# Optimization experiments

Hardware: AMD Instinct MI355X
Metric: run time of the kernel (lower is better)

## Reference

```python
import jax, jax.numpy as jnp
import numpy as np

NUM_HEADS = 16
NUM_GROUPS = 4
EPS = 1e-6


def _rope_tables(seq_len, head_dim):
    inv_freq = 1.0 / (10000.0 ** (jnp.arange(0, head_dim, 2, dtype=jnp.float32) / head_dim))
    t = jnp.arange(seq_len, dtype=jnp.float32)
    freqs = jnp.outer(t, inv_freq)  # [s, hd//2]
    return jnp.sin(freqs), jnp.cos(freqs)


def _apply_rope(x, sin, cos):
    # x: [b, s, h, hd]; sin/cos: [s, hd//2] -> broadcast over batch and heads
    sin = sin[None, :, None, :]
    cos = cos[None, :, None, :]
    x1 = x[..., ::2]
    x2 = x[..., 1::2]
    out1 = x1 * cos - x2 * sin
    out2 = x1 * sin + x2 * cos
    return jnp.stack([out1, out2], axis=-1).reshape(x.shape).astype(x.dtype)


def _rmsnorm(x, scale):
    var = jnp.mean(jnp.square(x), axis=-1, keepdims=True)
    return x * jax.lax.rsqrt(var + EPS) * scale


def setup_inputs() -> dict:
    key = jax.random.key(0)
    b, s, d = 16, 512, 2048
    hd = d // NUM_HEADS
    g = NUM_GROUPS
    ks = jax.random.split(key, 9)
    std = 0.02
    return {
        "x": jax.random.normal(ks[0], (b, s, d), dtype=jnp.float32),
        "Wq": jax.random.normal(ks[1], (d, d), dtype=jnp.float32) * std,
        "bq": jnp.zeros((d,), dtype=jnp.float32),
        "Wk": jax.random.normal(ks[2], (d, g * hd), dtype=jnp.float32) * std,
        "bk": jnp.zeros((g * hd,), dtype=jnp.float32),
        "Wv": jax.random.normal(ks[3], (d, g * hd), dtype=jnp.float32) * std,
        "bv": jnp.zeros((g * hd,), dtype=jnp.float32),
        "Wo": jax.random.normal(ks[4], (d, d), dtype=jnp.float32) * std,
        "bo": jnp.zeros((d,), dtype=jnp.float32),
        "q_norm_scale": jnp.ones((hd,), dtype=jnp.float32),
        "k_norm_scale": jnp.ones((hd,), dtype=jnp.float32),
    }


def reference(x, Wq, bq, Wk, bk, Wv, bv, Wo, bo, q_norm_scale, k_norm_scale):
    b, s, d = x.shape
    H, G = NUM_HEADS, NUM_GROUPS
    hd = d // H
    P = H // G  # queries per kv group
    inv_sqrt_hd = hd ** (-0.5)

    q = (x @ Wq + bq).reshape(b, s, H, hd)
    k = (x @ Wk + bk).reshape(b, s, G, hd)
    v = (x @ Wv + bv).reshape(b, s, G, hd)

    q = _rmsnorm(q, q_norm_scale)
    k = _rmsnorm(k, k_norm_scale)

    sin, cos = _rope_tables(s, hd)
    q = _apply_rope(q, sin, cos) * inv_sqrt_hd  # module pre-scales q
    k = _apply_rope(k, sin, cos)

    # GQA attention with causal mask; dot_product_attention applies an
    # additional 1/sqrt(hd) scale on top of the module's pre-scaling.
    qg = q.reshape(b, s, G, P, hd)
    logits = jnp.einsum("bsgph,btgh->bgpst", qg, k) * inv_sqrt_hd
    causal = jnp.tril(jnp.ones((s, s), dtype=bool))
    logits = jnp.where(causal[None, None, None, :, :], logits, jnp.finfo(logits.dtype).min)
    attn = jax.nn.softmax(logits, axis=-1)
    out = jnp.einsum("bgpst,btgh->bsgph", attn, v).reshape(b, s, d)
    return out @ Wo + bo
```

## Files before the change

kernel.cpp:

```cpp
#include <hip/hip_runtime.h>
#include <stdint.h>

typedef __attribute__((ext_vector_type(4))) float floatx4;
typedef __attribute__((ext_vector_type(16))) float floatx16;
typedef __attribute__((ext_vector_type(8))) short short8;

#define BB 16
#define SS 512
#define DD 2048
#define HH_ 16
#define HD 128
#define GG 4
#define MM (BB*SS)
#define NQKV 3072

__device__ __forceinline__ unsigned short f2bf(float f){
  unsigned u = __builtin_bit_cast(unsigned, f);
  u += 0x7fffu + ((u >> 16) & 1u);
  return (unsigned short)(u >> 16);
}
__device__ __forceinline__ float bf2f_lo(unsigned d){
  return __builtin_bit_cast(float, d << 16);
}
__device__ __forceinline__ float bf2f_hi(unsigned d){
  return __builtin_bit_cast(float, d & 0xffff0000u);
}

__device__ __forceinline__ void async_copy16(const void* g, void* l){
  __builtin_amdgcn_global_load_lds((const __attribute__((address_space(1))) unsigned*)g,
                                   (__attribute__((address_space(3))) unsigned*)l,
                                   16, 0, 0);
}

#define PB_CVT   16384
#define PB_TRQ   (PB_CVT + 4096)
#define PB_TRK   (PB_TRQ + 1024)
#define PB_TRV   (PB_TRK + 1024)
#define PB_TRO   (PB_TRV + 4096)
#define PB_ALL   (PB_TRO + 12)

__global__ __launch_bounds__(256) void prep_kernel(
    const float* __restrict__ x,
    const float* __restrict__ Wq, const float* __restrict__ Wk,
    const float* __restrict__ Wv, const float* __restrict__ Wo,
    const float* __restrict__ bq, const float* __restrict__ bk,
    const float* __restrict__ bv,
    unsigned short* __restrict__ xb, unsigned short* __restrict__ WqkvT,
    unsigned short* __restrict__ WoT, float* __restrict__ bqkv)
{
  __shared__ float tile[32][33];
  const int bid = blockIdx.x, tid = threadIdx.x;

  if (bid < PB_CVT) {
    const int i = bid * 256 + tid;
    float4 f = ((const float4*)x)[i];
    ushort4 o;
    o.x = f2bf(f.x); o.y = f2bf(f.y); o.z = f2bf(f.z); o.w = f2bf(f.w);
    ((ushort4*)xb)[i] = o;
    return;
  }
  if (bid < PB_TRO) {
    const float* src; unsigned short* dst; int R, C, b2;
    if (bid < PB_TRQ)      { src = Wq; dst = WqkvT;                          R = 2048; C = 2048; b2 = bid - PB_CVT; }
    else if (bid < PB_TRK) { src = Wk; dst = WqkvT + (size_t)2048 * 2048;    R = 2048; C = 512;  b2 = bid - PB_TRQ; }
    else if (bid < PB_TRV) { src = Wv; dst = WqkvT + (size_t)2560 * 2048;    R = 2048; C = 512;  b2 = bid - PB_TRK; }
    else                   { src = Wo; dst = WoT;                            R = 2048; C = 2048; b2 = bid - PB_TRV; }
    const int nbx = C >> 5;
    const int c0 = (b2 % nbx) * 32, r0 = (b2 / nbx) * 32;
    const int tx = tid & 31, ty = tid >> 5;
    #pragma unroll
    for (int j = 0; j < 32; j += 8)
      tile[ty + j][tx] = src[(size_t)(r0 + ty + j) * C + (c0 + tx)];
    __syncthreads();
    #pragma unroll
    for (int j = 0; j < 32; j += 8)
      dst[(size_t)(c0 + ty + j) * R + (r0 + tx)] = f2bf(tile[tx][ty + j]);
    return;
  }
  {
    const int i = (bid - PB_TRO) * 256 + tid;
    if (i < NQKV)
      bqkv[i] = (i < 2048) ? bq[i] : (i < 2560 ? bk[i - 2048] : bv[i - 2560]);
  }
}

template<bool OUT_BF16>
__global__ __launch_bounds__(256) void gemm_bt_kernel(
    const unsigned short* __restrict__ A,
    const unsigned short* __restrict__ Bt,
    void* __restrict__ Cout,
    const float* __restrict__ bias,
    int M, int N, int K, int ldc)
{
  __shared__ unsigned short sA[128 * 64];
  __shared__ unsigned short sB[128 * 64];
  const int tid  = threadIdx.x;
  const int wave = tid >> 6;
  const int lane = tid & 63;
  const int m0 = blockIdx.y * 128;
  const int n0 = blockIdx.x * 128;
  const int wm = (wave >> 1) * 64;
  const int wn = (wave & 1) * 64;

  floatx16 acc[2][2];
  #pragma unroll
  for (int i = 0; i < 2; i++)
    #pragma unroll
    for (int j = 0; j < 2; j++)
      #pragma unroll
      for (int r = 0; r < 16; r++) acc[i][j][r] = 0.f;

  const int sglog = (lane & 7) ^ ((lane >> 3) & 7);
  const unsigned short* gA = A  + (size_t)(m0 + 32 * wave + (lane >> 3)) * K + sglog * 8;
  const unsigned short* gB = Bt + (size_t)(n0 + 32 * wave + (lane >> 3)) * K + sglog * 8;
  unsigned short* lA = &sA[32 * wave * 64];
  unsigned short* lB = &sB[32 * wave * 64];

  for (int k0 = 0; k0 < K; k0 += 64) {
    #pragma unroll
    for (int c = 0; c < 4; ++c) {
      async_copy16(gA + (size_t)c * 8 * K + k0, lA + c * 512);
      async_copy16(gB + (size_t)c * 8 * K + k0, lB + c * 512);
    }
    __syncthreads();

    #pragma unroll
    for (int kh = 0; kh < 4; ++kh) {
      const int slot = (kh * 2 + (lane >> 5)) ^ (lane & 7);
      short8 aF[2], bF[2];
      #pragma unroll
      for (int i = 0; i < 2; ++i)
        aF[i] = *(const short8*)(&sA[(wm + i * 32 + (lane & 31)) * 64 + slot * 8]);
      #pragma unroll
      for (int j = 0; j < 2; ++j)
        bF[j] = *(const short8*)(&sB[(wn + j * 32 + (lane & 31)) * 64 + slot * 8]);
      #pragma unroll
      for (int i = 0; i < 2; ++i)
        #pragma unroll
        for (int j = 0; j < 2; ++j)
          acc[i][j] = __builtin_amdgcn_mfma_f32_32x32x16_bf16(aF[i], bF[j], acc[i][j], 0, 0, 0);
    }
    __syncthreads();
  }

  const int cc = lane & 31;
  const int rb = 4 * (lane >> 5);
  #pragma unroll
  for (int j = 0; j < 2; j++) {
    const int col = n0 + wn + j * 32 + cc;
    const float bval = bias[col];
    #pragma unroll
    for (int i = 0; i < 2; i++) {
      #pragma unroll
      for (int reg = 0; reg < 16; reg++) {
        const int row = m0 + wm + i * 32 + (reg & 3) + 8 * (reg >> 2) + rb;
        const float v = acc[i][j][reg] + bval;
        if (OUT_BF16)
          ((unsigned short*)Cout)[(size_t)row * ldc + col] = f2bf(v);
        else
          ((float*)Cout)[(size_t)row * ldc + col] = v;
      }
    }
  }
}

template<bool OUT_BF16>
__global__ __launch_bounds__(512, 2) void gemm256_kernel(
    const unsigned short* __restrict__ A,
    const unsigned short* __restrict__ Bt,
    void* __restrict__ Cout,
    const float* __restrict__ bias,
    int N, int K, int ldc)
{
  __shared__ unsigned short sA[4 * 128 * 64];
  __shared__ unsigned short sB[4 * 128 * 64];

  const int tid  = threadIdx.x;
  const int wave = tid >> 6, lane = tid & 63;
  const int wm = wave >> 2, wn = wave & 3;
  const int l15 = lane & 15, l7 = lane & 7, q4 = lane >> 4;

  const int nbn = N >> 8;
  const int cpx = gridDim.x >> 3;
  const int bid = (blockIdx.x & 7) * cpx + (blockIdx.x >> 3);
  const int m0 = (bid / nbn) * 256;
  const int n0 = (bid % nbn) * 256;

  const int rowOff = wave * 8 + (lane >> 3);
  const int glog   = l7 ^ ((lane >> 3) & 7);
  const unsigned short* gA = A  + (size_t)(m0 + rowOff) * K + glog * 8;
  const unsigned short* gB = Bt + (size_t)(n0 + rowOff) * K + glog * 8;

#define STAGE_A(j, tt) do { \
    unsigned short* d_ = &sA[(2 * ((tt) & 1) + (j)) * 8192 + wave * 512]; \
    const unsigned short* s_ = gA + (size_t)((j) * 128) * K + (tt) * 64; \
    async_copy16(s_, d_); \
    async_copy16(s_ + (size_t)64 * K, d_ + 4096); } while (0)
#define STAGE_B(j, tt) do { \
    unsigned short* d_ = &sB[(2 * ((tt) & 1) + (j)) * 8192 + wave * 512]; \
    const unsigned short* s_ = gB + (size_t)((j) * 128) * K + (tt) * 64; \
    async_copy16(s_, d_); \
    async_copy16(s_ + (size_t)64 * K, d_ + 4096); } while (0)
#define FENCE() asm volatile("" ::: "memory")
#define BAR()   do { FENCE(); __builtin_amdgcn_s_barrier(); FENCE(); } while (0)

  STAGE_B(0, 0); STAGE_B(1, 0); STAGE_A(0, 0); STAGE_A(1, 0);
  STAGE_B(0, 1); STAGE_B(1, 1); STAGE_A(0, 1); STAGE_A(1, 1);

  floatx4 acc[8][4];
  #pragma unroll
  for (int i = 0; i < 8; ++i)
    #pragma unroll
    for (int j = 0; j < 4; ++j)
      acc[i][j] = (floatx4){0.f, 0.f, 0.f, 0.f};

  asm volatile("s_waitcnt vmcnt(8)" ::: "memory");
  BAR();

  short8 aF[4][2], bF[4][2];
  const int NT = K >> 6;

  const unsigned short* pA = &sA[l15 * 64];
  const unsigned short* pB = &sB[((wn & 1) * 64 + l15) * 64];
  const int g0 = ((0 + q4) ^ l7) * 8;
  const int g1 = ((4 + q4) ^ l7) * 8;

#define LDA_(fa_, rb_, sa_) do { \
    aF[fa_][0] = *(const short8*)(pA + (sa_) * 8192 + ((rb_) + (fa_) * 16) * 64 + g0); \
    aF[fa_][1] = *(const short8*)(pA + (sa_) * 8192 + ((rb_) + (fa_) * 16) * 64 + g1); } while (0)
#define LDB_(fb_, sb_) do { \
    bF[fb_][0] = *(const short8*)(pB + (sb_) * 8192 + (fb_) * 16 * 64 + g0); \
    bF[fb_][1] = *(const short8*)(pB + (sb_) * 8192 + (fb_) * 16 * 64 + g1); } while (0)
#define MFMA_Q(fa0, fb0) \
    _Pragma("unroll") \
    for (int fa = 0; fa < 4; ++fa) { \
      _Pragma("unroll") \
      for (int fb = 0; fb < 2; ++fb) { \
        acc[(fa0)+fa][(fb0)+fb] = __builtin_amdgcn_mfma_f32_16x16x32_bf16(aF[fa][0], bF[(fb0)+fb][0], acc[(fa0)+fa][(fb0)+fb], 0, 0, 0); \
        acc[(fa0)+fa][(fb0)+fb] = __builtin_amdgcn_mfma_f32_16x16x32_bf16(aF[fa][1], bF[(fb0)+fb][1], acc[(fa0)+fa][(fb0)+fb], 0, 0, 0); \
      } \
    }

  #pragma unroll 1
  for (int t = 0; t < NT; ++t) {
    const int sa = 2 * (t & 1) + wm;
    const int sb = 2 * (t & 1) + (wn >> 1);
    LDB_(0, sb); LDB_(1, sb);
    LDA_(0, 0, sa); LDA_(1, 0, sa); LDA_(2, 0, sa); LDA_(3, 0, sa);
    __builtin_amdgcn_s_setprio(1);
    MFMA_Q(0, 0);
    __builtin_amdgcn_s_setprio(0);
    BAR();
    LDB_(2, sb); LDB_(3, sb);
    __builtin_amdgcn_s_setprio(1);
    MFMA_Q(0, 2);
    __builtin_amdgcn_s_setprio(0);
    BAR();
    LDA_(0, 64, sa); LDA_(1, 64, sa); LDA_(2, 64, sa); LDA_(3, 64, sa);
    if (t + 2 < NT) { STAGE_B(0, t + 2); STAGE_B(1, t + 2); }
    __builtin_amdgcn_s_setprio(1);
    MFMA_Q(4, 0);
    __builtin_amdgcn_s_setprio(0);
    BAR();
    if (t + 2 < NT) {
      STAGE_A(0, t + 2); STAGE_A(1, t + 2);
      asm volatile("s_waitcnt vmcnt(8)" ::: "memory");
    } else if (t + 1 < NT) {
      asm volatile("s_waitcnt vmcnt(0)" ::: "memory");
    }
    __builtin_amdgcn_s_setprio(1);
    MFMA_Q(4, 2);
    __builtin_amdgcn_s_setprio(0);
    BAR();
  }
#undef STAGE_A
#undef STAGE_B
#undef LDA_
#undef LDB_
#undef MFMA_Q
#undef FENCE
#undef BAR

  const int r4 = q4 * 4;
  #pragma unroll
  for (int fb = 0; fb < 4; ++fb) {
    const int col = n0 + wn * 64 + fb * 16 + l15;
    const float bval = bias[col];
    #pragma unroll
    for (int fa = 0; fa < 8; ++fa) {
      const size_t rowb = (size_t)(m0 + wm * 128 + fa * 16 + r4);
      #pragma unroll
      for (int r = 0; r < 4; ++r) {
        const float v = acc[fa][fb][r] + bval;
        if (OUT_BF16)
          ((unsigned short*)Cout)[(rowb + r) * ldc + col] = f2bf(v);
        else
          ((float*)Cout)[(rowb + r) * ldc + col] = v;
      }
    }
  }
}

__global__ __launch_bounds__(256) void norm_vtr_kernel(
    unsigned short* __restrict__ qkv,
    const float* __restrict__ qs, const float* __restrict__ ks,
    unsigned short* __restrict__ vt)
{
  __shared__ unsigned short tileV[32][34];
  const int bid = blockIdx.x, tid = threadIdx.x;

  if (bid < 40960) {
    const int wave = tid >> 6, lane = tid & 63;
    const int gw  = bid * 4 + wave;
    const int row = gw / 20;
    const int hh  = gw % 20;
    const bool isq = hh < 16;

    unsigned* p = (unsigned*)(qkv + (size_t)row * NQKV + hh * 128) + lane;
    unsigned d = *p;
    float x1 = bf2f_lo(d), x2 = bf2f_hi(d);

    float ss = x1 * x1 + x2 * x2;
    #pragma unroll
    for (int off = 32; off; off >>= 1) ss += __shfl_xor(ss, off, 64);
    const float r = rsqrtf(ss * (1.f / 128.f) + 1e-6f);

    const float2 sc = ((const float2*)(isq ? qs : ks))[lane];
    float n1 = x1 * r * sc.x;
    float n2 = x2 * r * sc.y;

    const float t = (float)(row & (SS - 1));
    const float freq = __expf((float)lane * (-2.f / 128.f) * 9.21034037197618f);
    float sn, cs;
    __sincosf(t * freq, &sn, &cs);
    float o1 = n1 * cs - n2 * sn;
    float o2 = n1 * sn + n2 * cs;
    if (isq) { o1 *= (1.f / 128.f); o2 *= (1.f / 128.f); }

    *p = (unsigned)f2bf(o1) | ((unsigned)f2bf(o2) << 16);
    return;
  }
  {
    const int b2 = bid - 40960;
    const int hd0 = (b2 & 3) * 32, t0 = ((b2 >> 2) & 15) * 32, bg = b2 >> 6;
    const int tx = tid & 31, ty = tid >> 5;
    const int b = bg >> 2, g = bg & 3;
    const unsigned short* src = qkv + (size_t)b * SS * NQKV + 2560 + g * HD;
    #pragma unroll
    for (int j = 0; j < 32; j += 8)
      tileV[ty + j][tx] = src[(size_t)(t0 + ty + j) * NQKV + hd0 + tx];
    __syncthreads();
    unsigned short* dst = vt + (size_t)bg * HD * SS;
    #pragma unroll
    for (int j = 0; j < 32; j += 8)
      dst[(size_t)(hd0 + ty + j) * SS + t0 + tx] = tileV[tx][ty + j];
  }
}

__global__ __launch_bounds__(512, 4) void fattn_kernel(
    const unsigned short* __restrict__ qkv,
    const unsigned short* __restrict__ vtb,
    unsigned short* __restrict__ aout)
{
  __shared__ unsigned short sK[2][64 * 128];
  __shared__ unsigned short sV[2][128 * 64];
  __shared__ unsigned short sP[8][16 * 64];

  const int lane = threadIdx.x & 63, wave = threadIdx.x >> 6;
  const int quad = lane >> 4, col = lane & 15;
  const int idx = blockIdx.x;
  const int qb = (0x1203 >> ((idx >> 8) * 4)) & 0xF;
  const int bh = idx & 255;
  const int b = bh >> 4, h = bh & 15, g = h >> 2;

  const int qrow = qb * 128 + wave * 16 + col;
  const unsigned short* qg = qkv + ((size_t)(b * SS + qrow)) * NQKV + h * HD + quad * 8;
  short8 qf[4];
  #pragma unroll
  for (int c = 0; c < 4; ++c) qf[c] = *(const short8*)(qg + c * 32);

  const unsigned short* kg = qkv + (size_t)b * SS * NQKV + 2048 + g * HD;
  const unsigned short* vg = vtb + ((size_t)(b * GG + g)) * HD * SS;

  floatx4 acc_o[8];
  #pragma unroll
  for (int i = 0; i < 8; ++i) acc_o[i] = (floatx4){0.f, 0.f, 0.f, 0.f};
  float m[4] = {-INFINITY, -INFINITY, -INFINITY, -INFINITY};
  float l[4] = {0.f, 0.f, 0.f, 0.f};

#define STAGE_KV(kt_, bf_) do { \
    const int t0_ = (kt_) * 64; \
    _Pragma("unroll") \
    for (int c = 0; c < 2; ++c) { \
      const int ci = c * 8 + wave; \
      { const int r_  = ci * 4 + (lane >> 4); \
        const int gl_ = (lane & 15) ^ (r_ & 15); \
        async_copy16(kg + (size_t)(t0_ + r_) * NQKV + gl_ * 8, &sK[bf_][ci * 512]); } \
      { const int r_  = ci * 8 + (lane >> 3); \
        const int gl_ = (lane & 7) ^ (r_ & 7); \
        async_copy16(vg + (size_t)r_ * SS + t0_ + gl_ * 8, &sV[bf_][ci * 512]); } \
    } } while (0)

  const int nkt = 2 * qb + 2;
  STAGE_KV(0, 0);

  for (int kt = 0; kt < nkt; ++kt) {
    const int buf = kt & 1;
    __syncthreads();
    if (kt + 1 < nkt) STAGE_KV(kt + 1, buf ^ 1);

    floatx4 sc[4];
    #pragma unroll
    for (int s = 0; s < 4; ++s) sc[s] = (floatx4){0.f, 0.f, 0.f, 0.f};
    __builtin_amdgcn_s_setprio(1);
    #pragma unroll
    for (int s = 0; s < 4; ++s) {
      const int trow = s * 16 + col;
      #pragma unroll
      for (int c = 0; c < 4; ++c) {
        const int p = (c * 4 + quad) ^ (trow & 15);
        const short8 kf = *(const short8*)(&sK[buf][trow * 128 + p * 8]);
        sc[s] = __builtin_amdgcn_mfma_f32_16x16x32_bf16(qf[c], kf, sc[s], 0, 0, 0);
      }
    }
    __builtin_amdgcn_s_setprio(0);

    if (kt >= 2 * qb) {
      #pragma unroll
      for (int s = 0; s < 4; ++s)
        #pragma unroll
        for (int r = 0; r < 4; ++r)
          if (kt * 64 + s * 16 + col > qb * 128 + wave * 16 + quad * 4 + r)
            sc[s][r] = -1e30f;
    }

    float mx[4], alpha[4], lsum[4];
    #pragma unroll
    for (int r = 0; r < 4; ++r) {
      mx[r] = fmaxf(fmaxf(sc[0][r], sc[1][r]), fmaxf(sc[2][r], sc[3][r]));
      #pragma unroll
      for (int off = 8; off; off >>= 1) mx[r] = fmaxf(mx[r], __shfl_xor(mx[r], off, 16));
      mx[r] = fmaxf(mx[r], m[r]);
      alpha[r] = __expf(m[r] - mx[r]);
      m[r] = mx[r];
      lsum[r] = 0.f;
    }
    #pragma unroll
    for (int s = 0; s < 4; ++s)
      #pragma unroll
      for (int r = 0; r < 4; ++r) {
        const float p = __expf(sc[s][r] - m[r]);
        lsum[r] += p;
        const int row = quad * 4 + r;
        const int slot = (s * 2 + (col >> 3)) ^ (row & 7);
        sP[wave][row * 64 + slot * 8 + (col & 7)] = f2bf(p);
      }
    #pragma unroll
    for (int r = 0; r < 4; ++r) {
      #pragma unroll
      for (int off = 8; off; off >>= 1) lsum[r] += __shfl_xor(lsum[r], off, 16);
      l[r] = l[r] * alpha[r] + lsum[r];
    }
    #pragma unroll
    for (int n = 0; n < 8; ++n)
      #pragma unroll
      for (int r = 0; r < 4; ++r) acc_o[n][r] *= alpha[r];

    short8 pf[2];
    #pragma unroll
    for (int kc = 0; kc < 2; ++kc)
      pf[kc] = *(const short8*)(&sP[wave][col * 64 + ((kc * 4 + quad) ^ (col & 7)) * 8]);
    __builtin_amdgcn_s_setprio(1);
    #pragma unroll
    for (int n = 0; n < 8; ++n) {
      const int hdrow = n * 16 + col;
      #pragma unroll
      for (int kc = 0; kc < 2; ++kc) {
        const int p = (kc * 4 + quad) ^ (hdrow & 7);
        const short8 vf = *(const short8*)(&sV[buf][hdrow * 64 + p * 8]);
        acc_o[n] = __builtin_amdgcn_mfma_f32_16x16x32_bf16(pf[kc], vf, acc_o[n], 0, 0, 0);
      }
    }
    __builtin_amdgcn_s_setprio(0);
  }
#undef STAGE_KV

  float inv[4];
  #pragma unroll
  for (int r = 0; r < 4; ++r) inv[r] = 1.f / l[r];
  unsigned short* ob = aout + ((size_t)(b * SS + qb * 128 + wave * 16)) * DD + h * HD;
  #pragma unroll
  for (int n = 0; n < 8; ++n)
    #pragma unroll
    for (int r = 0; r < 4; ++r)
      ob[(size_t)(quad * 4 + r) * DD + n * 16 + col] = f2bf(acc_o[n][r] * inv[r]);
}

extern "C" void kernel_launch(void* const* d_in, const int* in_sizes, int n_in,
                              void* d_out, int out_size, void* d_ws, size_t ws_size,
                              hipStream_t stream) {
  const float* x   = (const float*)d_in[0];
  const float* Wq  = (const float*)d_in[1];
  const float* bq  = (const float*)d_in[2];
  const float* Wk  = (const float*)d_in[3];
  const float* bk  = (const float*)d_in[4];
  const float* Wv  = (const float*)d_in[5];
  const float* bv  = (const float*)d_in[6];
  const float* Wo  = (const float*)d_in[7];
  const float* bo  = (const float*)d_in[8];
  const float* qns = (const float*)d_in[9];
  const float* kns = (const float*)d_in[10];

  char* ws = (char*)d_ws;
  unsigned short* xb    = (unsigned short*)(ws);
  unsigned short* vtb   = (unsigned short*)(ws);
  unsigned short* WqkvT = (unsigned short*)(ws + 33554432);
  unsigned short* WoT   = (unsigned short*)(ws + 46137344);
  float*          bqkv  = (float*)         (ws + 54525952);
  unsigned short* qkv   = (unsigned short*)(ws + 54538240);
  unsigned short* aout  = (unsigned short*)(ws + 104869888);

  prep_kernel<<<PB_ALL, 256, 0, stream>>>(x, Wq, Wk, Wv, Wo, bq, bk, bv,
                                          xb, WqkvT, WoT, bqkv);
  gemm_bt_kernel<true><<<dim3(24, 64), 256, 0, stream>>>(xb, WqkvT, qkv, bqkv,
                                                         MM, NQKV, DD, NQKV);
  norm_vtr_kernel<<<45056, 256, 0, stream>>>(qkv, qns, kns, vtb);
  fattn_kernel<<<1024, 512, 0, stream>>>(qkv, vtb, aout);
  gemm256_kernel<false><<<256, 512, 0, stream>>>(aout, WoT, d_out, bo,
                                                 DD, DD, DD);
  (void)in_sizes; (void)n_in; (void)out_size; (void)ws_size;
}
```

Before: 409.7 us.

## Fuse QK RMSNorm and RoPE into QKV GEMM epilogue with precomputed table

Moves the per-head RMSNorm and rotary embedding for Q and K into the QKV GEMM epilogue, reducing the separate normalization kernel to only the V transpose. The epilogue computes per-row sums of squares across the 128-wide head tile using shuffles and a shared-memory combine, then applies the scale and RoPE using a cos/sin table precomputed in the prep kernel. This removes a full read-modify-write pass over the Q/K part of the qkv buffer. In exchange the GEMM epilogue gains shuffles, a barrier and table loads, which raises register pressure. The table is placed in the aout workspace region, which is safe only because attention writes aout after the GEMM has finished reading it.

```diff
diff --git a/kernel.cpp b/kernel.cpp
--- a/kernel.cpp
+++ b/kernel.cpp
@@ -37,7 +37,8 @@
 #define PB_TRK   (PB_TRQ + 1024)
 #define PB_TRV   (PB_TRK + 1024)
 #define PB_TRO   (PB_TRV + 4096)
-#define PB_ALL   (PB_TRO + 12)
+#define PB_BIAS  (PB_TRO + 12)
+#define PB_ALL   (PB_BIAS + 128)
 
 __global__ __launch_bounds__(256) void prep_kernel(
     const float* __restrict__ x,
@@ -46,7 +47,8 @@
     const float* __restrict__ bq, const float* __restrict__ bk,
     const float* __restrict__ bv,
     unsigned short* __restrict__ xb, unsigned short* __restrict__ WqkvT,
-    unsigned short* __restrict__ WoT, float* __restrict__ bqkv)
+    unsigned short* __restrict__ WoT, float* __restrict__ bqkv,
+    float* __restrict__ ropetab)
 {
   __shared__ float tile[32][33];
   const int bid = blockIdx.x, tid = threadIdx.x;
@@ -77,19 +79,29 @@
       dst[(size_t)(c0 + ty + j) * R + (r0 + tx)] = f2bf(tile[tx][ty + j]);
     return;
   }
-  {
+  if (bid < PB_BIAS) {
     const int i = (bid - PB_TRO) * 256 + tid;
     if (i < NQKV)
       bqkv[i] = (i < 2048) ? bq[i] : (i < 2560 ? bk[i - 2048] : bv[i - 2560]);
-  }
-}
-
-template<bool OUT_BF16>
-__global__ __launch_bounds__(256) void gemm_bt_kernel(
+    return;
+  }
+  {
+    const int idx = (bid - PB_BIAS) * 256 + tid;
+    const int fi = idx >> 9, t = idx & 511;
+    const float freq = __expf((float)fi * (-2.f / 128.f) * 9.21034037197618f);
+    float sn, cs;
+    __sincosf((float)t * freq, &sn, &cs);
+    ((float2*)ropetab)[idx] = make_float2(cs, sn);
+  }
+}
+
+__global__ __launch_bounds__(256) void gemm_qkv_kernel(
     const unsigned short* __restrict__ A,
     const unsigned short* __restrict__ Bt,
-    void* __restrict__ Cout,
+    unsigned short* __restrict__ Cout,
     const float* __restrict__ bias,
+    const float* __restrict__ qs, const float* __restrict__ ks,
+    const float* __restrict__ ropetab,
     int M, int N, int K, int ldc)
 {
   __shared__ unsigned short sA[128 * 64];
@@ -145,21 +157,77 @@
 
   const int cc = lane & 31;
   const int rb = 4 * (lane >> 5);
+
   #pragma unroll
   for (int j = 0; j < 2; j++) {
-    const int col = n0 + wn + j * 32 + cc;
-    const float bval = bias[col];
+    const float bval = bias[n0 + wn + j * 32 + cc];
+    #pragma unroll
+    for (int i = 0; i < 2; i++)
+      #pragma unroll
+      for (int reg = 0; reg < 16; reg++)
+        acc[i][j][reg] += bval;
+  }
+
+  if (n0 < 2560) {
+    float* sums = (float*)sA;
+    #pragma unroll
+    for (int i = 0; i < 2; i++)
+      #pragma unroll
+      for (int reg = 0; reg < 16; reg++) {
+        float p = acc[i][0][reg] * acc[i][0][reg] + acc[i][1][reg] * acc[i][1][reg];
+        #pragma unroll
+        for (int off = 1; off < 32; off <<= 1) p += __shfl_xor(p, off, 32);
+        if (cc == 0)
+          sums[(wn >> 6) * 128 + wm + i * 32 + (reg & 3) + 8 * (reg >> 2) + rb] = p;
+      }
+    __syncthreads();
+
+    const float* scale = (n0 < 2048) ? qs : ks;
+    const float sc0 = scale[wn + cc], sc1 = scale[wn + 32 + cc];
+    const float osc = (n0 < 2048) ? (1.f / 128.f) : 1.f;
+    const float sgn = (lane & 1) ? 1.f : -1.f;
+    const int fi0 = (wn + cc) >> 1, fi1 = (wn + 32 + cc) >> 1;
+
     #pragma unroll
     for (int i = 0; i < 2; i++) {
       #pragma unroll
-      for (int reg = 0; reg < 16; reg++) {
-        const int row = m0 + wm + i * 32 + (reg & 3) + 8 * (reg >> 2) + rb;
-        const float v = acc[i][j][reg] + bval;
-        if (OUT_BF16)
-          ((unsigned short*)Cout)[(size_t)row * ldc + col] = f2bf(v);
-        else
-          ((float*)Cout)[(size_t)row * ldc + col] = v;
+      for (int q = 0; q < 4; q++) {
+        const int lr0 = wm + i * 32 + 8 * q + rb;
+        float rms[4];
+        #pragma unroll
+        for (int r = 0; r < 4; r++)
+          rms[r] = rsqrtf((sums[lr0 + r] + sums[128 + lr0 + r]) * (1.f / 128.f) + 1e-6f);
+        const int t0i = (m0 + lr0) & (SS - 1);
+        #pragma unroll
+        for (int j = 0; j < 2; j++) {
+          const int fi = j ? fi1 : fi0;
+          const float4* tp = (const float4*)(ropetab + (size_t)(fi * 512 + t0i) * 2);
+          const float4 tA = tp[0], tB = tp[1];
+          const float csv[4] = {tA.x, tA.z, tB.x, tB.z};
+          const float snv[4] = {tA.y, tA.w, tB.y, tB.w};
+          const float scj = j ? sc1 : sc0;
+          #pragma unroll
+          for (int r = 0; r < 4; r++) {
+            const int reg = q * 4 + r;
+            float nv = acc[i][j][reg] * rms[r] * scj;
+            float pv = __shfl_xor(nv, 1, 64);
+            float o = (nv * csv[r] + sgn * pv * snv[r]) * osc;
+            Cout[(size_t)(m0 + lr0 + r) * ldc + (n0 + wn + j * 32 + cc)] = f2bf(o);
+          }
+        }
       }
+    }
+  } else {
+    #pragma unroll
+    for (int j = 0; j < 2; j++) {
+      const int col = n0 + wn + j * 32 + cc;
+      #pragma unroll
+      for (int i = 0; i < 2; i++)
+        #pragma unroll
+        for (int reg = 0; reg < 16; reg++) {
+          const int row = m0 + wm + i * 32 + (reg & 3) + 8 * (reg >> 2) + rb;
+          Cout[(size_t)row * ldc + col] = f2bf(acc[i][j][reg]);
+        }
     }
   }
 }
@@ -301,60 +369,24 @@
   }
 }
 
-__global__ __launch_bounds__(256) void norm_vtr_kernel(
-    unsigned short* __restrict__ qkv,
-    const float* __restrict__ qs, const float* __restrict__ ks,
+__global__ __launch_bounds__(256) void vtr_kernel(
+    const unsigned short* __restrict__ qkv,
     unsigned short* __restrict__ vt)
 {
   __shared__ unsigned short tileV[32][34];
-  const int bid = blockIdx.x, tid = threadIdx.x;
-
-  if (bid < 40960) {
-    const int wave = tid >> 6, lane = tid & 63;
-    const int gw  = bid * 4 + wave;
-    const int row = gw / 20;
-    const int hh  = gw % 20;
-    const bool isq = hh < 16;
-
-    unsigned* p = (unsigned*)(qkv + (size_t)row * NQKV + hh * 128) + lane;
-    unsigned d = *p;
-    float x1 = bf2f_lo(d), x2 = bf2f_hi(d);
-
-    float ss = x1 * x1 + x2 * x2;
-    #pragma unroll
-    for (int off = 32; off; off >>= 1) ss += __shfl_xor(ss, off, 64);
-    const float r = rsqrtf(ss * (1.f / 128.f) + 1e-6f);
-
-    const float2 sc = ((const float2*)(isq ? qs : ks))[lane];
-    float n1 = x1 * r * sc.x;
-    float n2 = x2 * r * sc.y;
-
-    const float t = (float)(row & (SS - 1));
-    const float freq = __expf((float)lane * (-2.f / 128.f) * 9.21034037197618f);
-    float sn, cs;
-    __sincosf(t * freq, &sn, &cs);
-    float o1 = n1 * cs - n2 * sn;
-    float o2 = n1 * sn + n2 * cs;
-    if (isq) { o1 *= (1.f / 128.f); o2 *= (1.f / 128.f); }
-
-    *p = (unsigned)f2bf(o1) | ((unsigned)f2bf(o2) << 16);
-    return;
-  }
-  {
-    const int b2 = bid - 40960;
-    const int hd0 = (b2 & 3) * 32, t0 = ((b2 >> 2) & 15) * 32, bg = b2 >> 6;
-    const int tx = tid & 31, ty = tid >> 5;
-    const int b = bg >> 2, g = bg & 3;
-    const unsigned short* src = qkv + (size_t)b * SS * NQKV + 2560 + g * HD;
-    #pragma unroll
-    for (int j = 0; j < 32; j += 8)
-      tileV[ty + j][tx] = src[(size_t)(t0 + ty + j) * NQKV + hd0 + tx];
-    __syncthreads();
-    unsigned short* dst = vt + (size_t)bg * HD * SS;
-    #pragma unroll
-    for (int j = 0; j < 32; j += 8)
-      dst[(size_t)(hd0 + ty + j) * SS + t0 + tx] = tileV[tx][ty + j];
-  }
+  const int b2 = blockIdx.x, tid = threadIdx.x;
+  const int hd0 = (b2 & 3) * 32, t0 = ((b2 >> 2) & 15) * 32, bg = b2 >> 6;
+  const int tx = tid & 31, ty = tid >> 5;
+  const int b = bg >> 2, g = bg & 3;
+  const unsigned short* src = qkv + (size_t)b * SS * NQKV + 2560 + g * HD;
+  #pragma unroll
+  for (int j = 0; j < 32; j += 8)
+    tileV[ty + j][tx] = src[(size_t)(t0 + ty + j) * NQKV + hd0 + tx];
+  __syncthreads();
+  unsigned short* dst = vt + (size_t)bg * HD * SS;
+  #pragma unroll
+  for (int j = 0; j < 32; j += 8)
+    dst[(size_t)(hd0 + ty + j) * SS + t0 + tx] = tileV[tx][ty + j];
 }
 
 __global__ __launch_bounds__(512, 4) void fattn_kernel(
@@ -519,12 +551,14 @@
   float*          bqkv  = (float*)         (ws + 54525952);
   unsigned short* qkv   = (unsigned short*)(ws + 54538240);
   unsigned short* aout  = (unsigned short*)(ws + 104869888);
+  float*          ropetab = (float*)(ws + 104869888);
 
   prep_kernel<<<PB_ALL, 256, 0, stream>>>(x, Wq, Wk, Wv, Wo, bq, bk, bv,
-                                          xb, WqkvT, WoT, bqkv);
-  gemm_bt_kernel<true><<<dim3(24, 64), 256, 0, stream>>>(xb, WqkvT, qkv, bqkv,
-                                                         MM, NQKV, DD, NQKV);
-  norm_vtr_kernel<<<45056, 256, 0, stream>>>(qkv, qns, kns, vtb);
+                                          xb, WqkvT, WoT, bqkv, ropetab);
+  gemm_qkv_kernel<<<dim3(24, 64), 256, 0, stream>>>(xb, WqkvT, qkv, bqkv,
+                                                    qns, kns, ropetab,
+                                                    MM, NQKV, DD, NQKV);
+  vtr_kernel<<<4096, 256, 0, stream>>>(qkv, vtb);
   fattn_kernel<<<1024, 512, 0, stream>>>(qkv, vtb, aout);
   gemm256_kernel<false><<<256, 512, 0, stream>>>(aout, WoT, d_out, bo,
                                                  DD, DD, DD);
```

Measured after the change: 427.1 us. 1.04x slower.
